# Kernel tuning notes

Measured on AMD Instinct MI355X. Metric: run time of the kernel, lower is better.

## Reference

```python
import jax, jax.numpy as jnp
import numpy as np

B, N, D, H, F = 2, 2048, 1024, 16, 4096
E = D // H
EPS = 1e-5

def layer_norm(x, g, b):
    mu = jnp.mean(x, axis=-1, keepdims=True)
    var = jnp.var(x, axis=-1, keepdims=True)
    return (x - mu) * jax.lax.rsqrt(var + EPS) * g + b

def setup_inputs() -> dict:
    key = jax.random.key(0)
    ks = jax.random.split(key, 16)
    s = lambda k, sh, fan: jax.random.normal(k, sh, jnp.float32) * (1.0 / np.sqrt(fan))
    return {
        'x': jax.random.normal(ks[0], (B, N, D), jnp.float32),
        'wq': s(ks[1], (D, D), D), 'bq': jnp.zeros((D,), jnp.float32),
        'wk': s(ks[2], (D, D), D), 'bk': jnp.zeros((D,), jnp.float32),
        'wv': s(ks[3], (D, D), D), 'bv': jnp.zeros((D,), jnp.float32),
        'w1': s(ks[4], (F, D), D), 'b1': jnp.zeros((F,), jnp.float32),
        'ln_mlp_g': jnp.ones((F,), jnp.float32), 'ln_mlp_b': jnp.zeros((F,), jnp.float32),
        'w2': s(ks[5], (D, F), F), 'b2': jnp.zeros((D,), jnp.float32),
        'ln1_g': jnp.ones((D,), jnp.float32), 'ln1_b': jnp.zeros((D,), jnp.float32),
        'ln2_g': jnp.ones((D,), jnp.float32), 'ln2_b': jnp.zeros((D,), jnp.float32),
    }

def reference(x, wq, bq, wk, bk, wv, bv, w1, b1, ln_mlp_g, ln_mlp_b, w2, b2, ln1_g, ln1_b, ln2_g, ln2_b):
    h = layer_norm(x, ln1_g, ln1_b)                       # [B,N,D]
    q = (h @ wq.T + bq).reshape(B, N, H, E).transpose(0, 2, 1, 3)  # [B,H,N,E]
    k = (h @ wk.T + bk).reshape(B, N, H, E).transpose(0, 2, 1, 3)
    v = (h @ wv.T + bv).reshape(B, N, H, E).transpose(0, 2, 1, 3)
    # faithful to source: score = q@k^T / sqrt(1/emb_dim) == q@k^T * sqrt(emb_dim)
    score = jnp.einsum('bhne,bhme->bhnm', q, k) * np.sqrt(D).astype(np.float32)
    causal = jnp.tril(jnp.ones((N, N), bool))
    score = jnp.where(causal[None, None], score, -jnp.inf)
    weight = jax.nn.softmax(score, axis=-1)
    attn = jnp.einsum('bhnm,bhme->bhne', weight, v)       # [B,H,N,E]
    attn = attn.transpose(0, 2, 1, 3).reshape(B, N, D)
    x = x + attn
    h2 = layer_norm(x, ln2_g, ln2_b)
    m = h2 @ w1.T + b1                                    # [B,N,F]
    m = jax.nn.relu(layer_norm(m, ln_mlp_g, ln_mlp_b))
    # faithful: no second residual in the source forward
    return m @ w2.T + b2
```

## Files before the change

### kernel.cpp

```cpp
#include <hip/hip_runtime.h>
#include <cstdint>

typedef __bf16 bf16_t;
typedef bf16_t bf16x8 __attribute__((ext_vector_type(8)));
typedef bf16_t bf16x4 __attribute__((ext_vector_type(4)));
typedef float  floatx4 __attribute__((ext_vector_type(4)));

#define GLD_LDS(g, l) __builtin_amdgcn_global_load_lds( \
    (const __attribute__((address_space(1))) unsigned int*)(g), \
    (__attribute__((address_space(3))) unsigned int*)(l), 16, 0, 0)

#define MFMA_BF16_16x16x32 __builtin_amdgcn_mfma_f32_16x16x32_bf16

__global__ __launch_bounds__(256) void prep(
    const float* __restrict__ wq, const float* __restrict__ wk,
    const float* __restrict__ wv, const float* __restrict__ w1,
    const float* __restrict__ w2, const float* __restrict__ bq,
    const float* __restrict__ bk,
    bf16_t* __restrict__ wqk_hi, bf16_t* __restrict__ wqk_lo,
    bf16_t* __restrict__ wvb, bf16_t* __restrict__ w1b, bf16_t* __restrict__ w2b,
    float* __restrict__ bqk) {
  const int blk = blockIdx.x, tid = threadIdx.x;
  if (blk < 2048) {
    const int qk = blk >> 10;
    const int i  = (blk & 1023) * 256 + tid;
    const float* src = qk ? wk : wq;
    float4 v = ((const float4*)src)[i];
    float f[4] = {v.x, v.y, v.z, v.w};
    bf16x4 h, l;
    #pragma unroll
    for (int j = 0; j < 4; ++j) { h[j] = (bf16_t)f[j]; l[j] = (bf16_t)(f[j] - (float)h[j]); }
    ((bf16x4*)(wqk_hi + qk * 1024 * 1024))[i] = h;
    ((bf16x4*)(wqk_lo + qk * 1024 * 1024))[i] = l;
  } else if (blk < 3072) {
    const int i = (blk - 2048) * 256 + tid;
    float4 v = ((const float4*)wv)[i];
    bf16x4 o; o[0]=(bf16_t)v.x; o[1]=(bf16_t)v.y; o[2]=(bf16_t)v.z; o[3]=(bf16_t)v.w;
    ((bf16x4*)wvb)[i] = o;
  } else if (blk < 7168) {
    const int i = (blk - 3072) * 256 + tid;
    float4 v = ((const float4*)w1)[i];
    bf16x4 o; o[0]=(bf16_t)v.x; o[1]=(bf16_t)v.y; o[2]=(bf16_t)v.z; o[3]=(bf16_t)v.w;
    ((bf16x4*)w1b)[i] = o;
  } else if (blk < 11264) {
    const int i = (blk - 7168) * 256 + tid;
    float4 v = ((const float4*)w2)[i];
    bf16x4 o; o[0]=(bf16_t)v.x; o[1]=(bf16_t)v.y; o[2]=(bf16_t)v.z; o[3]=(bf16_t)v.w;
    ((bf16x4*)w2b)[i] = o;
  } else {
    const int i = (blk - 11264) * 256 + tid;
    if (i < 1024) { bqk[i] = bq[i]; bqk[1024 + i] = bk[i]; }
  }
}


__device__ __forceinline__ void block_sum2(float& s, float& ss, float* red) {
  #pragma unroll
  for (int off = 32; off > 0; off >>= 1) {
    s  += __shfl_down(s, off);
    ss += __shfl_down(ss, off);
  }
  const int wave = threadIdx.x >> 6;
  if ((threadIdx.x & 63) == 0) { red[wave * 2] = s; red[wave * 2 + 1] = ss; }
  __syncthreads();
  s  = red[0] + red[2] + red[4] + red[6];
  ss = red[1] + red[3] + red[5] + red[7];
}

__global__ __launch_bounds__(256) void ln_fwd_split(const float* __restrict__ x,
    const float* __restrict__ g, const float* __restrict__ b,
    bf16_t* __restrict__ out_hi, bf16_t* __restrict__ out_lo) {
  __shared__ float red[8];
  const size_t row = blockIdx.x;
  float4 v = ((const float4*)(x + row * 1024))[threadIdx.x];
  float s  = v.x + v.y + v.z + v.w;
  float ss = v.x*v.x + v.y*v.y + v.z*v.z + v.w*v.w;
  block_sum2(s, ss, red);
  const float mu  = s * (1.f / 1024.f);
  const float var = ss * (1.f / 1024.f) - mu * mu;
  const float rs  = rsqrtf(var + 1e-5f);
  float4 gg = ((const float4*)g)[threadIdx.x];
  float4 bb = ((const float4*)b)[threadIdx.x];
  float f[4];
  f[0] = (v.x - mu) * rs * gg.x + bb.x;
  f[1] = (v.y - mu) * rs * gg.y + bb.y;
  f[2] = (v.z - mu) * rs * gg.z + bb.z;
  f[3] = (v.w - mu) * rs * gg.w + bb.w;
  bf16x4 oh, ol;
  #pragma unroll
  for (int j = 0; j < 4; ++j) {
    oh[j] = (bf16_t)f[j];
    ol[j] = (bf16_t)(f[j] - (float)oh[j]);
  }
  ((bf16x4*)(out_hi + row * 1024))[threadIdx.x] = oh;
  ((bf16x4*)(out_lo + row * 1024))[threadIdx.x] = ol;
}

__global__ __launch_bounds__(256) void resid_ln_fwd(const float* __restrict__ x,
    const float* __restrict__ a, const float* __restrict__ g, const float* __restrict__ b,
    bf16_t* __restrict__ out) {
  __shared__ float red[8];
  const size_t row = blockIdx.x;
  float4 v = ((const float4*)(x + row * 1024))[threadIdx.x];
  float4 av = ((const float4*)(a + row * 1024))[threadIdx.x];
  v.x += av.x; v.y += av.y; v.z += av.z; v.w += av.w;
  float s  = v.x + v.y + v.z + v.w;
  float ss = v.x*v.x + v.y*v.y + v.z*v.z + v.w*v.w;
  block_sum2(s, ss, red);
  const float mu  = s * (1.f / 1024.f);
  const float var = ss * (1.f / 1024.f) - mu * mu;
  const float rs  = rsqrtf(var + 1e-5f);
  float4 gg = ((const float4*)g)[threadIdx.x];
  float4 bb = ((const float4*)b)[threadIdx.x];
  bf16x4 o;
  o[0] = (bf16_t)((v.x - mu) * rs * gg.x + bb.x);
  o[1] = (bf16_t)((v.y - mu) * rs * gg.y + bb.y);
  o[2] = (bf16_t)((v.z - mu) * rs * gg.z + bb.z);
  o[3] = (bf16_t)((v.w - mu) * rs * gg.w + bb.w);
  ((bf16x4*)(out + row * 1024))[threadIdx.x] = o;
}

__global__ __launch_bounds__(256) void ln_relu_inplace(bf16_t* __restrict__ m,
    const float* __restrict__ g, const float* __restrict__ b) {
  __shared__ float red[8];
  const size_t row = blockIdx.x;
  bf16_t* mr = m + row * 4096;
  const int base = threadIdx.x * 16;
  bf16x8 v0 = *(bf16x8*)(mr + base);
  bf16x8 v1 = *(bf16x8*)(mr + base + 8);
  float f[16];
  #pragma unroll
  for (int i = 0; i < 8; ++i) { f[i] = (float)v0[i]; f[8 + i] = (float)v1[i]; }
  float s = 0.f, ss = 0.f;
  #pragma unroll
  for (int i = 0; i < 16; ++i) { s += f[i]; ss += f[i] * f[i]; }
  block_sum2(s, ss, red);
  const float mu  = s * (1.f / 4096.f);
  const float var = ss * (1.f / 4096.f) - mu * mu;
  const float rs  = rsqrtf(var + 1e-5f);
  bf16x8 o0, o1;
  #pragma unroll
  for (int i = 0; i < 16; ++i) {
    float ov = (f[i] - mu) * rs * g[base + i] + b[base + i];
    ov = fmaxf(ov, 0.f);
    if (i < 8) o0[i] = (bf16_t)ov; else o1[i - 8] = (bf16_t)ov;
  }
  *(bf16x8*)(mr + base) = o0;
  *(bf16x8*)(mr + base + 8) = o1;
}

__device__ __forceinline__ void xcd_chunk2d(int& bx, int& by) {
  const int gx = gridDim.x;
  const int f  = (int)(blockIdx.y * gx + blockIdx.x);
  const int xcd = f & 7;
  const int i = f >> 3;
  const int bxPer = gx >> 3;
  by = i / bxPer;
  bx = xcd * bxPer + (i - by * bxPer);
}

template <int OUT_MODE, int BM, int SK, int BK>
__global__ __launch_bounds__(256) void gemm_bt(
    const bf16_t* __restrict__ A, const bf16_t* __restrict__ Bw,
    const float* __restrict__ bias, void* __restrict__ Cp,
    int M, int N, int K) {
  constexpr int MI = BM / 32;
  constexpr bool DB = (BK == 32);
  constexpr int ASZ = BM * BK;
  constexpr int BSZ = 128 * BK;
  __shared__ bf16_t As[(DB ? 2 : 1) * ASZ];
  __shared__ bf16_t Bs[(DB ? 2 : 1) * BSZ];
  const int tid  = threadIdx.x;
  const int wave = tid >> 6, lane = tid & 63;
  const int quad = lane >> 4, l15 = lane & 15;
  int bx = blockIdx.x, by = blockIdx.y;
  xcd_chunk2d(bx, by);
  const int m0 = bx * BM, n0 = by * 128;
  const int wm = (wave >> 1) * (BM / 2), wn = (wave & 1) * 64;
  const int ks = (SK > 1) ? (int)blockIdx.z : 0;
  const int kbeg = ks * (K / SK), kend = kbeg + K / SK;

  floatx4 acc[MI][4] = {};

  if constexpr (BK == 32) {
    const int srowA = wave * (BM / 4) + (lane >> 2);
    const int srowB = wave * 32 + (lane >> 2);
    const int scol = (lane & 3) * 8;
    const bf16_t* Ag = A  + (size_t)(m0 + srowA) * K + scol;
    const bf16_t* Bg = Bw + (size_t)(n0 + srowB) * K + scol;
    auto stage = [&](int buf, int k0) {
      #pragma unroll
      for (int i = 0; i < BM / 64; ++i)
        GLD_LDS(Ag + (size_t)(i * 16) * K + k0,
                As + buf * ASZ + wave * (BM / 4) * 32 + i * 512);
      #pragma unroll
      for (int i = 0; i < 2; ++i)
        GLD_LDS(Bg + (size_t)(i * 16) * K + k0,
                Bs + buf * BSZ + wave * 1024 + i * 512);
    };
    stage(0, kbeg);
    __syncthreads();
    int cur = 0;
    for (int k0 = kbeg; k0 < kend; k0 += 32) {
      if (k0 + 32 < kend) stage(cur ^ 1, k0 + 32);
      bf16x8 af[MI], bfr[4];
      #pragma unroll
      for (int i = 0; i < MI; ++i)
        af[i] = *(const bf16x8*)(As + cur * ASZ + (wm + i * 16 + l15) * 32 + quad * 8);
      #pragma unroll
      for (int j = 0; j < 4; ++j)
        bfr[j] = *(const bf16x8*)(Bs + cur * BSZ + (wn + j * 16 + l15) * 32 + quad * 8);
      #pragma unroll
      for (int i = 0; i < MI; ++i)
        #pragma unroll
        for (int j = 0; j < 4; ++j)
          acc[i][j] = MFMA_BF16_16x16x32(af[i], bfr[j], acc[i][j], 0, 0, 0);
      __syncthreads();
      cur ^= 1;
    }
  } else {
    for (int k0 = kbeg; k0 < kend; k0 += 64) {
      __syncthreads();
      #pragma unroll
      for (int i = 0; i < BM / 32; ++i) {
        const int flat = i * 64 + lane;
        const int rl = flat >> 3, ch = flat & 7;
        GLD_LDS(A + (size_t)(m0 + wave * (BM / 4) + rl) * K + k0 + ((ch ^ (rl & 7)) * 8),
                As + wave * (BM / 4) * 64 + i * 512);
      }
      #pragma unroll
      for (int i = 0; i < 4; ++i) {
        const int flat = i * 64 + lane;
        const int rl = flat >> 3, ch = flat & 7;
        GLD_LDS(Bw + (size_t)(n0 + wave * 32 + rl) * K + k0 + ((ch ^ (rl & 7)) * 8),
                Bs + wave * 32 * 64 + i * 512);
      }
      __syncthreads();
      #pragma unroll
      for (int kk = 0; kk < 2; ++kk) {
        const int co = ((quad + 4 * kk) ^ (l15 & 7)) * 8;
        bf16x8 af[MI], bfr[4];
        #pragma unroll
        for (int i = 0; i < MI; ++i)
          af[i] = *(const bf16x8*)(As + (wm + i * 16 + l15) * 64 + co);
        #pragma unroll
        for (int j = 0; j < 4; ++j)
          bfr[j] = *(const bf16x8*)(Bs + (wn + j * 16 + l15) * 64 + co);
        #pragma unroll
        for (int i = 0; i < MI; ++i)
          #pragma unroll
          for (int j = 0; j < 4; ++j)
            acc[i][j] = MFMA_BF16_16x16x32(af[i], bfr[j], acc[i][j], 0, 0, 0);
      }
    }
  }

  if (OUT_MODE == 3) {
    #pragma unroll
    for (int j = 0; j < 4; ++j) {
      const int col = n0 + wn + j * 16 + l15;
      const float bv = bias[col];
      const int h = col >> 6, e = col & 63;
      #pragma unroll
      for (int i = 0; i < MI; ++i) {
        const int row0 = m0 + wm + i * 16 + quad * 4;
        const int b = row0 >> 11, n = row0 & 2047;
        bf16x4 o;
        #pragma unroll
        for (int r = 0; r < 4; ++r) o[r] = (bf16_t)(acc[i][j][r] + bv);
        *(bf16x4*)((bf16_t*)Cp + ((size_t)((b << 4) + h) * 64 + e) * 2048 + n) = o;
      }
    }
    return;
  }
  #pragma unroll
  for (int j = 0; j < 4; ++j) {
    const int col = n0 + wn + j * 16 + l15;
    const float bv = (SK == 1 || ks == 0) ? bias[col] : 0.f;
    #pragma unroll
    for (int i = 0; i < MI; ++i) {
      #pragma unroll
      for (int r = 0; r < 4; ++r) {
        const int row = m0 + wm + i * 16 + quad * 4 + r;
        const float v = acc[i][j][r] + bv;
        if (OUT_MODE == 0) {
          if (SK > 1) atomicAdd(&((float*)Cp)[(size_t)row * N + col], v);
          else        ((float*)Cp)[(size_t)row * N + col] = v;
        } else if (OUT_MODE == 1) {
          ((bf16_t*)Cp)[(size_t)row * N + col] = (bf16_t)v;
        }
      }
    }
  }
}

__global__ __launch_bounds__(256) void gemm_qk_split(
    const bf16_t* __restrict__ Ah, const bf16_t* __restrict__ Al,
    const bf16_t* __restrict__ Bh, const bf16_t* __restrict__ Bl,
    const float* __restrict__ bias,
    bf16_t* __restrict__ qhi, bf16_t* __restrict__ qlo,
    bf16_t* __restrict__ khi, bf16_t* __restrict__ klo,
    int M, int N, int K) {
  __shared__ bf16_t Ash[64 * 64];
  __shared__ bf16_t Asl[64 * 64];
  __shared__ bf16_t Bsh[128 * 64];
  __shared__ bf16_t Bsl[128 * 64];
  const int tid  = threadIdx.x;
  const int wave = tid >> 6, lane = tid & 63;
  const int quad = lane >> 4, l15 = lane & 15;
  int bx = blockIdx.x, by = blockIdx.y;
  xcd_chunk2d(bx, by);
  const int m0 = bx * 64, n0 = by * 128;
  const int wm = (wave >> 1) * 32, wn = (wave & 1) * 64;

  floatx4 acc[2][4] = {};

  for (int k0 = 0; k0 < K; k0 += 64) {
    __syncthreads();
    #pragma unroll
    for (int i = 0; i < 2; ++i) {
      const int flat = i * 64 + lane;
      const int rl = flat >> 3, ch = flat & 7;
      const size_t off = (size_t)(m0 + wave * 16 + rl) * K + k0 + ((ch ^ (rl & 7)) * 8);
      GLD_LDS(Ah + off, Ash + wave * 16 * 64 + i * 512);
      GLD_LDS(Al + off, Asl + wave * 16 * 64 + i * 512);
    }
    #pragma unroll
    for (int i = 0; i < 4; ++i) {
      const int flat = i * 64 + lane;
      const int rl = flat >> 3, ch = flat & 7;
      const size_t off = (size_t)(n0 + wave * 32 + rl) * K + k0 + ((ch ^ (rl & 7)) * 8);
      GLD_LDS(Bh + off, Bsh + wave * 32 * 64 + i * 512);
      GLD_LDS(Bl + off, Bsl + wave * 32 * 64 + i * 512);
    }
    __syncthreads();
    #pragma unroll
    for (int kk = 0; kk < 2; ++kk) {
      const int co = ((quad + 4 * kk) ^ (l15 & 7)) * 8;
      bf16x8 ah[2], al[2], bh[4], bl[4];
      #pragma unroll
      for (int i = 0; i < 2; ++i) {
        const int ro = (wm + i * 16 + l15) * 64 + co;
        ah[i] = *(const bf16x8*)(Ash + ro);
        al[i] = *(const bf16x8*)(Asl + ro);
      }
      #pragma unroll
      for (int j = 0; j < 4; ++j) {
        const int ro = (wn + j * 16 + l15) * 64 + co;
        bh[j] = *(const bf16x8*)(Bsh + ro);
        bl[j] = *(const bf16x8*)(Bsl + ro);
      }
      #pragma unroll
      for (int i = 0; i < 2; ++i)
        #pragma unroll
        for (int j = 0; j < 4; ++j) {
          acc[i][j] = MFMA_BF16_16x16x32(ah[i], bh[j], acc[i][j], 0, 0, 0);
          acc[i][j] = MFMA_BF16_16x16x32(ah[i], bl[j], acc[i][j], 0, 0, 0);
          acc[i][j] = MFMA_BF16_16x16x32(al[i], bh[j], acc[i][j], 0, 0, 0);
        }
    }
  }
  #pragma unroll
  for (int j = 0; j < 4; ++j) {
    const int col = n0 + wn + j * 16 + l15;
    const float bv = bias[col];
    const bool isq = col < 1024;
    bf16_t* hib = isq ? qhi : khi;
    bf16_t* lob = isq ? qlo : klo;
    const float scale = isq ? 32.0f : 1.0f;
    const int h = (col >> 6) & 15, e = col & 63;
    #pragma unroll
    for (int i = 0; i < 2; ++i) {
      #pragma unroll
      for (int r = 0; r < 4; ++r) {
        const int row = m0 + wm + i * 16 + quad * 4 + r;
        const int b = row >> 11, n = row & 2047;
        const float c = (acc[i][j][r] + bv) * scale;
        const bf16_t chi = (bf16_t)c;
        const bf16_t clo = (bf16_t)(c - (float)chi);
        const size_t dst = (((size_t)((b << 4) + h) * 2048 + n) << 6) + e;
        hib[dst] = chi;
        lob[dst] = clo;
      }
    }
  }
}

#define SWZ(row, chunk) (((row) << 6) + ((((chunk) ^ ((row) & 7))) << 3))
__global__ __launch_bounds__(256, 4) void attn_causal(
    const bf16_t* __restrict__ qhi, const bf16_t* __restrict__ qlo,
    const bf16_t* __restrict__ khi, const bf16_t* __restrict__ klo,
    const bf16_t* __restrict__ vT, float* __restrict__ o) {
  __shared__ bf16_t KsH[64 * 64];
  __shared__ bf16_t KsL[64 * 64];
  __shared__ bf16_t Vt[64 * 64];
  __shared__ bf16_t Ps[4][16 * 64];

  const int tid  = threadIdx.x;
  const int wave = tid >> 6, lane = tid & 63;
  const int quad = lane >> 4, l15 = lane & 15;
  const int bh = blockIdx.x;
  const int q0 = (31 - (int)blockIdx.y) * 64;
  const size_t hb = (size_t)bh * 2048;

  const int wmin = q0 + wave * 16;
  const int qrow = wmin + l15;
  bf16x8 qh[2], ql[2];
  {
    const bf16_t* qbh = qhi + ((hb + wmin + l15) << 6) + quad * 8;
    const bf16_t* qbl = qlo + ((hb + wmin + l15) << 6) + quad * 8;
    qh[0] = *(const bf16x8*)qbh;
    qh[1] = *(const bf16x8*)(qbh + 32);
    ql[0] = *(const bf16x8*)qbl;
    ql[1] = *(const bf16x8*)(qbl + 32);
  }

  floatx4 accO[4] = {};
  float m_row = -1e30f;
  float l_row = 0.f;

  const int kr = wave * 16 + (lane >> 3);
  const int kc7 = lane & 7;
  const bf16_t* kgh = khi + ((hb + kr) << 6) + kc7 * 8;
  const bf16_t* kgl = klo + ((hb + kr) << 6) + kc7 * 8;
  const bf16_t* vg  = vT + ((size_t)(bh * 64 + kr)) * 2048 + kc7 * 8;

  bf16x8 pkh0 = *(const bf16x8*)(kgh);
  bf16x8 pkh1 = *(const bf16x8*)(kgh + (8 << 6));
  bf16x8 pkl0 = *(const bf16x8*)(kgl);
  bf16x8 pkl1 = *(const bf16x8*)(kgl + (8 << 6));
  bf16x8 pv0  = *(const bf16x8*)(vg);
  bf16x8 pv1  = *(const bf16x8*)(vg + 8 * 2048);

  const int ntiles = (q0 >> 6) + 1;
  for (int t = 0; t < ntiles; ++t) {
    const int k0 = t * 64;
    __syncthreads();
    *(bf16x8*)(KsH + SWZ(kr, kc7))     = pkh0;
    *(bf16x8*)(KsH + SWZ(kr + 8, kc7)) = pkh1;
    *(bf16x8*)(KsL + SWZ(kr, kc7))     = pkl0;
    *(bf16x8*)(KsL + SWZ(kr + 8, kc7)) = pkl1;
    *(bf16x8*)(Vt  + SWZ(kr, kc7))     = pv0;
    *(bf16x8*)(Vt  + SWZ(kr + 8, kc7)) = pv1;
    if (t + 1 < ntiles) {
      const int koff = (t + 1) << 12;
      pkh0 = *(const bf16x8*)(kgh + koff);
      pkh1 = *(const bf16x8*)(kgh + koff + (8 << 6));
      pkl0 = *(const bf16x8*)(kgl + koff);
      pkl1 = *(const bf16x8*)(kgl + koff + (8 << 6));
      pv0  = *(const bf16x8*)(vg + (t + 1) * 64);
      pv1  = *(const bf16x8*)(vg + (t + 1) * 64 + 8 * 2048);
    }
    __syncthreads();

    const bool needmask = (k0 + 63 > wmin);

    floatx4 sv[4];
    __builtin_amdgcn_s_setprio(1);
    #pragma unroll
    for (int j = 0; j < 4; ++j) {
      const int rK = j * 16 + l15;
      const bf16x8 kh0 = *(const bf16x8*)(KsH + SWZ(rK, quad));
      const bf16x8 kh1 = *(const bf16x8*)(KsH + SWZ(rK, quad + 4));
      const bf16x8 kl0 = *(const bf16x8*)(KsL + SWZ(rK, quad));
      const bf16x8 kl1 = *(const bf16x8*)(KsL + SWZ(rK, quad + 4));
      floatx4 acc = {};
      acc = MFMA_BF16_16x16x32(kh0, qh[0], acc, 0, 0, 0);
      acc = MFMA_BF16_16x16x32(kh1, qh[1], acc, 0, 0, 0);
      acc = MFMA_BF16_16x16x32(kl0, qh[0], acc, 0, 0, 0);
      acc = MFMA_BF16_16x16x32(kl1, qh[1], acc, 0, 0, 0);
      acc = MFMA_BF16_16x16x32(kh0, ql[0], acc, 0, 0, 0);
      acc = MFMA_BF16_16x16x32(kh1, ql[1], acc, 0, 0, 0);
      sv[j] = acc;
    }
    __builtin_amdgcn_s_setprio(0);

    const int lim = qrow - k0 - quad * 4;
    float mr = -1e30f;
    #pragma unroll
    for (int j = 0; j < 4; ++j)
      #pragma unroll
      for (int r = 0; r < 4; ++r) {
        float x = sv[j][r];
        if (needmask && (j * 16 + r > lim)) x = -1e30f;
        sv[j][r] = x;
        mr = fmaxf(mr, x);
      }
    mr = fmaxf(mr, __shfl_xor(mr, 16));
    mr = fmaxf(mr, __shfl_xor(mr, 32));
    const float mold = m_row;
    const float mnew = fmaxf(mold, mr);
    m_row = mnew;
    float psum = 0.f;
    bf16x4 pb[4];
    #pragma unroll
    for (int j = 0; j < 4; ++j)
      #pragma unroll
      for (int r = 0; r < 4; ++r) {
        const float p = __expf(sv[j][r] - mnew);
        const bf16_t pv = (bf16_t)p;
        psum += (float)pv;
        pb[j][r] = pv;
      }
    {
      bf16_t* pw = &Ps[wave][0];
      #pragma unroll
      for (int j = 0; j < 4; ++j)
        *(bf16x4*)(pw + SWZ(l15, 2 * j + (quad >> 1)) + (quad & 1) * 4) = pb[j];
    }
    psum += __shfl_xor(psum, 16);
    psum += __shfl_xor(psum, 32);
    const float alpha = __expf(mold - mnew);
    l_row = l_row * alpha + psum;
    if (__any(mnew > mold)) {
      #pragma unroll
      for (int r = 0; r < 4; ++r) {
        const float ar = __shfl(alpha, quad * 4 + r);
        #pragma unroll
        for (int j = 0; j < 4; ++j) accO[j][r] *= ar;
      }
    }
    asm volatile("s_waitcnt lgkmcnt(0)" ::: "memory");
    __builtin_amdgcn_sched_barrier(0);

    bf16x8 pf[2];
    {
      const bf16_t* pw = &Ps[wave][0];
      pf[0] = *(const bf16x8*)(pw + SWZ(l15, quad));
      pf[1] = *(const bf16x8*)(pw + SWZ(l15, quad + 4));
    }
    __builtin_amdgcn_s_setprio(1);
    #pragma unroll
    for (int j = 0; j < 4; ++j) {
      const int rV = j * 16 + l15;
      const bf16x8 vf0 = *(const bf16x8*)(Vt + SWZ(rV, quad));
      const bf16x8 vf1 = *(const bf16x8*)(Vt + SWZ(rV, quad + 4));
      accO[j] = MFMA_BF16_16x16x32(pf[0], vf0, accO[j], 0, 0, 0);
      accO[j] = MFMA_BF16_16x16x32(pf[1], vf1, accO[j], 0, 0, 0);
    }
    __builtin_amdgcn_s_setprio(0);
  }

  const int b = bh >> 4, h = bh & 15;
  #pragma unroll
  for (int r = 0; r < 4; ++r) {
    const float lr = __shfl(l_row, quad * 4 + r);
    const float linv = 1.f / lr;
    const int qr = wmin + quad * 4 + r;
    float* orow = o + ((size_t)(b * 2048) + qr) * 1024 + h * 64;
    #pragma unroll
    for (int j = 0; j < 4; ++j)
      orow[j * 16 + l15] = accO[j][r] * linv;
  }
}


extern "C" void kernel_launch(void* const* d_in, const int* in_sizes, int n_in,
                              void* d_out, int out_size, void* d_ws, size_t ws_size,
                              hipStream_t stream) {
  const float* x        = (const float*)d_in[0];
  const float* wq       = (const float*)d_in[1];
  const float* bq       = (const float*)d_in[2];
  const float* wk       = (const float*)d_in[3];
  const float* bk       = (const float*)d_in[4];
  const float* wv       = (const float*)d_in[5];
  const float* bv       = (const float*)d_in[6];
  const float* w1       = (const float*)d_in[7];
  const float* b1       = (const float*)d_in[8];
  const float* ln_mlp_g = (const float*)d_in[9];
  const float* ln_mlp_b = (const float*)d_in[10];
  const float* w2       = (const float*)d_in[11];
  const float* b2       = (const float*)d_in[12];
  const float* ln1_g    = (const float*)d_in[13];
  const float* ln1_b    = (const float*)d_in[14];
  const float* ln2_g    = (const float*)d_in[15];
  const float* ln2_b    = (const float*)d_in[16];

  char* ws = (char*)d_ws;
  bf16_t* h_hi   = (bf16_t*)(ws);
  bf16_t* h_lo   = (bf16_t*)(ws + (8u  << 20));
  bf16_t* wqk_hi = (bf16_t*)(ws + (16u << 20));
  bf16_t* wqk_lo = (bf16_t*)(ws + (20u << 20));
  bf16_t* wvb    = (bf16_t*)(ws + (24u << 20));
  float*  bqk    = (float*) (ws + (26u << 20));
  bf16_t* w1b    = (bf16_t*)(ws + (28u << 20));
  bf16_t* w2b    = (bf16_t*)(ws + (36u << 20));
  bf16_t* qhi    = (bf16_t*)(ws + (44u << 20));
  bf16_t* qlo    = (bf16_t*)(ws + (52u << 20));
  bf16_t* khi    = (bf16_t*)(ws + (60u << 20));
  bf16_t* klo    = (bf16_t*)(ws + (68u << 20));
  bf16_t* mbuf   = (bf16_t*)(ws + (44u << 20));
  bf16_t* vTb    = (bf16_t*)(ws + (76u << 20));
  float*  attnb  = (float*) (ws + (84u << 20));
  bf16_t* h2     = (bf16_t*)(ws + (100u << 20));

  hipMemsetAsync(d_out, 0, (size_t)4096 * 1024 * sizeof(float), stream);

  prep<<<11268, 256, 0, stream>>>(wq, wk, wv, w1, w2, bq, bk,
                                  wqk_hi, wqk_lo, wvb, w1b, w2b, bqk);

  ln_fwd_split<<<4096, 256, 0, stream>>>(x, ln1_g, ln1_b, h_hi, h_lo);
  gemm_qk_split<<<dim3(64, 16), 256, 0, stream>>>(h_hi, h_lo, wqk_hi, wqk_lo, bqk,
                                                  qhi, qlo, khi, klo, 4096, 2048, 1024);
  gemm_bt<3, 64, 1, 64><<<dim3(64, 8), 256, 0, stream>>>(h_hi, wvb, bv, vTb, 4096, 1024, 1024);
  attn_causal<<<dim3(32, 32), 256, 0, stream>>>(qhi, qlo, khi, klo, vTb, attnb);
  resid_ln_fwd<<<4096, 256, 0, stream>>>(x, attnb, ln2_g, ln2_b, h2);
  gemm_bt<1, 128, 1, 64><<<dim3(32, 32), 256, 0, stream>>>(h2, w1b, b1, mbuf, 4096, 4096, 1024);
  ln_relu_inplace<<<4096, 256, 0, stream>>>(mbuf, ln_mlp_g, ln_mlp_b);
  gemm_bt<0, 64, 2, 64><<<dim3(64, 8, 2), 256, 0, stream>>>(mbuf, w2b, b2, d_out, 4096, 1024, 4096);

  (void)in_sizes; (void)n_in; (void)out_size; (void)ws_size;
}
```

Baseline: 411.3 us.

## Fold log2e into Q scale, compute row sums via MFMA, retune W1 GEMM

Q is now prescaled by 32*log2(e), so the softmax can use exp2f instead of __expf. The row-sum reduction moves from per-lane accumulation plus cross-lane shuffles to an MFMA of P against a ones vector, and the rescale of l_row joins the accO rescale. The W1 GEMM template's last tile parameter changes from 64 to 32. Row sums are now taken from the bf16-rounded P values that are written to shared memory, and the larger Q scale may change bf16 hi/lo splitting accuracy slightly.

```diff
diff --git a/kernel.cpp b/kernel.cpp
--- a/kernel.cpp
+++ b/kernel.cpp
@@ -367,7 +367,7 @@
     const bool isq = col < 1024;
     bf16_t* hib = isq ? qhi : khi;
     bf16_t* lob = isq ? qlo : klo;
-    const float scale = isq ? 32.0f : 1.0f;
+    const float scale = isq ? 46.166241f : 1.0f;
     const int h = (col >> 6) & 15, e = col & 63;
     #pragma unroll
     for (int i = 0; i < 2; ++i) {
@@ -414,10 +414,13 @@
     ql[0] = *(const bf16x8*)qbl;
     ql[1] = *(const bf16x8*)(qbl + 32);
   }
+  bf16x8 onesf;
+  #pragma unroll
+  for (int i = 0; i < 8; ++i) onesf[i] = (bf16_t)1.0f;
 
   floatx4 accO[4] = {};
   float m_row = -1e30f;
-  float l_row = 0.f;
+  float l_rowD[4] = {};
 
   const int kr = wave * 16 + (lane >> 3);
   const int kc7 = lane & 7;
@@ -476,50 +479,36 @@
     __builtin_amdgcn_s_setprio(0);
 
     const int lim = qrow - k0 - quad * 4;
-    float mr = -1e30f;
-    #pragma unroll
-    for (int j = 0; j < 4; ++j)
+    float mj[4];
+    #pragma unroll
+    for (int j = 0; j < 4; ++j) {
       #pragma unroll
       for (int r = 0; r < 4; ++r) {
         float x = sv[j][r];
         if (needmask && (j * 16 + r > lim)) x = -1e30f;
         sv[j][r] = x;
-        mr = fmaxf(mr, x);
-      }
+      }
+      mj[j] = fmaxf(fmaxf(sv[j][0], sv[j][1]), fmaxf(sv[j][2], sv[j][3]));
+    }
+    float mr = fmaxf(fmaxf(mj[0], mj[1]), fmaxf(mj[2], mj[3]));
     mr = fmaxf(mr, __shfl_xor(mr, 16));
     mr = fmaxf(mr, __shfl_xor(mr, 32));
     const float mold = m_row;
     const float mnew = fmaxf(mold, mr);
     m_row = mnew;
-    float psum = 0.f;
     bf16x4 pb[4];
     #pragma unroll
     for (int j = 0; j < 4; ++j)
       #pragma unroll
-      for (int r = 0; r < 4; ++r) {
-        const float p = __expf(sv[j][r] - mnew);
-        const bf16_t pv = (bf16_t)p;
-        psum += (float)pv;
-        pb[j][r] = pv;
-      }
+      for (int r = 0; r < 4; ++r)
+        pb[j][r] = (bf16_t)exp2f(sv[j][r] - mnew);
     {
       bf16_t* pw = &Ps[wave][0];
       #pragma unroll
       for (int j = 0; j < 4; ++j)
         *(bf16x4*)(pw + SWZ(l15, 2 * j + (quad >> 1)) + (quad & 1) * 4) = pb[j];
     }
-    psum += __shfl_xor(psum, 16);
-    psum += __shfl_xor(psum, 32);
-    const float alpha = __expf(mold - mnew);
-    l_row = l_row * alpha + psum;
-    if (__any(mnew > mold)) {
-      #pragma unroll
-      for (int r = 0; r < 4; ++r) {
-        const float ar = __shfl(alpha, quad * 4 + r);
-        #pragma unroll
-        for (int j = 0; j < 4; ++j) accO[j][r] *= ar;
-      }
-    }
+    const float alpha = exp2f(mold - mnew);
     asm volatile("s_waitcnt lgkmcnt(0)" ::: "memory");
     __builtin_amdgcn_sched_barrier(0);
 
@@ -529,6 +518,22 @@
       pf[0] = *(const bf16x8*)(pw + SWZ(l15, quad));
       pf[1] = *(const bf16x8*)(pw + SWZ(l15, quad + 4));
     }
+    floatx4 ps = {};
+    ps = MFMA_BF16_16x16x32(pf[0], onesf, ps, 0, 0, 0);
+    ps = MFMA_BF16_16x16x32(pf[1], onesf, ps, 0, 0, 0);
+    if (__any(mnew > mold)) {
+      #pragma unroll
+      for (int r = 0; r < 4; ++r) {
+        const float ar = __shfl(alpha, quad * 4 + r);
+        l_rowD[r] = l_rowD[r] * ar + ps[r];
+        #pragma unroll
+        for (int j = 0; j < 4; ++j) accO[j][r] *= ar;
+      }
+    } else {
+      #pragma unroll
+      for (int r = 0; r < 4; ++r) l_rowD[r] += ps[r];
+    }
+
     __builtin_amdgcn_s_setprio(1);
     #pragma unroll
     for (int j = 0; j < 4; ++j) {
@@ -544,8 +549,7 @@
   const int b = bh >> 4, h = bh & 15;
   #pragma unroll
   for (int r = 0; r < 4; ++r) {
-    const float lr = __shfl(l_row, quad * 4 + r);
-    const float linv = 1.f / lr;
+    const float linv = 1.f / l_rowD[r];
     const int qr = wmin + quad * 4 + r;
     float* orow = o + ((size_t)(b * 2048) + qr) * 1024 + h * 64;
     #pragma unroll
@@ -605,7 +609,7 @@
   gemm_bt<3, 64, 1, 64><<<dim3(64, 8), 256, 0, stream>>>(h_hi, wvb, bv, vTb, 4096, 1024, 1024);
   attn_causal<<<dim3(32, 32), 256, 0, stream>>>(qhi, qlo, khi, klo, vTb, attnb);
   resid_ln_fwd<<<4096, 256, 0, stream>>>(x, attnb, ln2_g, ln2_b, h2);
-  gemm_bt<1, 128, 1, 64><<<dim3(32, 32), 256, 0, stream>>>(h2, w1b, b1, mbuf, 4096, 4096, 1024);
+  gemm_bt<1, 128, 1, 32><<<dim3(32, 32), 256, 0, stream>>>(h2, w1b, b1, mbuf, 4096, 4096, 1024);
   ln_relu_inplace<<<4096, 256, 0, stream>>>(mbuf, ln_mlp_g, ln_mlp_b);
   gemm_bt<0, 64, 2, 64><<<dim3(64, 8, 2), 256, 0, stream>>>(mbuf, w2b, b2, d_out, 4096, 1024, 4096);
 
```

New measurement: 400.3 us. 2.7% less time.
